# Kernel optimization log

Measured on AMD Instinct MI355X. Metric: run time of the kernel, lower is better.

Reference implementation:

```python
import jax, jax.numpy as jnp
import numpy as np

HIDDEN = 16
N_CLASSES = 10
N_NODES = 100000
N_EDGES = 3200000
D_FEAT = 128
NEG_SLOPE = 0.1


def setup_inputs() -> dict:
    key = jax.random.key(0)
    k1, k2, k3 = jax.random.split(key, 3)
    features = jax.random.normal(k1, (N_NODES, D_FEAT), dtype=jnp.float32)
    edge_src = jax.random.randint(k2, (N_EDGES,), 0, N_NODES, dtype=jnp.int64)
    edge_dst = jax.random.randint(k3, (N_EDGES,), 0, N_NODES, dtype=jnp.int64)
    return {"features": features, "edge_src": edge_src, "edge_dst": edge_dst}


def reference(features, edge_src, edge_dst):
    # SpMM: h[v] = sum over edges (u->v) of features[u]   (binary adjacency)
    msgs = features[edge_src]                      # [E, F] irregular gather
    h = jax.ops.segment_sum(msgs, edge_dst, num_segments=N_NODES)  # [N, F]
    # x @ ones(F, HIDDEN): every column equals the row-sum of h
    r1 = jnp.sum(h, axis=-1)                       # [N]
    a1 = jax.nn.leaky_relu(r1, NEG_SLOPE)          # leaky relu, slope 0.1
    # x @ ones(HIDDEN, N_CLASSES): each class column = HIDDEN * a1
    r2 = HIDDEN * a1
    a2 = jax.nn.leaky_relu(r2, NEG_SLOPE)
    # x @ ones(N_CLASSES, 1) then .int() and flatten
    r3 = N_CLASSES * a2                            # [N]
    return r3.astype(jnp.int32).reshape(-1)
```

## Files before the change

kernel.cpp:

```cpp
#include <hip/hip_runtime.h>

#define N_NODES  100000
#define N_EDGES  3200000
#define D_FEAT   128
#define SLICE    33344
#define SLICE4   (SLICE / 4)
#define N_SLICES 3
#define NCHUNK   80
#define EPB      40000
#define TPB      1024
#define STRIDE   (TPB * 8)

__device__ __forceinline__ unsigned short f2bf(float f) {
    union { float f; unsigned u; } c; c.f = f;
    unsigned r = c.u + 0x7FFFu + ((c.u >> 16) & 1u);
    return (unsigned short)(r >> 16);
}
__device__ __forceinline__ float bf2f(unsigned short h) {
    union { unsigned u; float f; } c; c.u = ((unsigned)h) << 16; return c.f;
}

__global__ void __launch_bounds__(256) rowsum_kernel(
    const float* __restrict__ feat,
    float* __restrict__ rowsum)
{
    const int gid = (int)(blockIdx.x * blockDim.x + threadIdx.x);
    const int row = gid >> 5;
    const int sub = gid & 31;
    if (row >= N_NODES) return;

    const float4 v = reinterpret_cast<const float4*>(
        feat + (size_t)row * D_FEAT)[sub];
    float s = (v.x + v.y) + (v.z + v.w);

    #pragma unroll
    for (int off = 16; off > 0; off >>= 1)
        s += __shfl_xor(s, off, 64);

    if (sub == 0) rowsum[row] = s;
}

__global__ void __launch_bounds__(256) gather_kernel(
    const int* __restrict__ edge_src,
    const float* __restrict__ rowsum,
    unsigned short* __restrict__ val)
{
    const int e = ((int)(blockIdx.x * 256 + threadIdx.x)) * 4;
    const int4 s4 = *reinterpret_cast<const int4*>(edge_src + e);
    ushort4 o;
    o.x = f2bf(rowsum[s4.x]);
    o.y = f2bf(rowsum[s4.y]);
    o.z = f2bf(rowsum[s4.z]);
    o.w = f2bf(rowsum[s4.w]);
    *reinterpret_cast<ushort4*>(val + e) = o;
}

__global__ void __launch_bounds__(TPB) scatter2_kernel(
    const int* __restrict__ edge_dst,
    const unsigned short* __restrict__ val,
    unsigned short* __restrict__ copies)
{
    __shared__ float lds[SLICE];

    const int tid = (int)threadIdx.x;
    const int bid = (int)blockIdx.x;
    const int g   = bid / 24;
    const int r   = bid % 24;
    const int xcd = r & 7;
    const int s   = r >> 3;
    const int b   = g * 8 + xcd;
    const int lo  = s * SLICE;
    const unsigned len = (unsigned)((N_NODES - lo < SLICE) ? (N_NODES - lo) : SLICE);

    float4 z; z.x = z.y = z.z = z.w = 0.0f;
    for (int i = tid; i < SLICE4; i += TPB)
        reinterpret_cast<float4*>(lds)[i] = z;
    __syncthreads();

    const int begin = b * EPB;
    const int end   = begin + EPB;

    int e = begin + tid * 8;
    bool v = (e < end);

    int4    d0, d1;
    ushort4 w01;
    ushort4 w23;
    if (v) {
        d0  = *(const int4*)(edge_dst + e);
        d1  = *(const int4*)(edge_dst + e + 4);
        w01 = *(const ushort4*)(val + e);
        w23 = *(const ushort4*)(val + e + 4);
    }

    while (v) {
        const int en = e + STRIDE;
        const bool vn = (en < end);
        int4 nd0, nd1; ushort4 nw01, nw23;
        if (vn) {
            nd0  = *(const int4*)(edge_dst + en);
            nd1  = *(const int4*)(edge_dst + en + 4);
            nw01 = *(const ushort4*)(val + en);
            nw23 = *(const ushort4*)(val + en + 4);
        }

        const unsigned j0 = (unsigned)(d0.x - lo);
        const unsigned j1 = (unsigned)(d0.y - lo);
        const unsigned j2 = (unsigned)(d0.z - lo);
        const unsigned j3 = (unsigned)(d0.w - lo);
        const unsigned j4 = (unsigned)(d1.x - lo);
        const unsigned j5 = (unsigned)(d1.y - lo);
        const unsigned j6 = (unsigned)(d1.z - lo);
        const unsigned j7 = (unsigned)(d1.w - lo);

        if (j0 < len) atomicAdd(&lds[j0], bf2f(w01.x));
        if (j1 < len) atomicAdd(&lds[j1], bf2f(w01.y));
        if (j2 < len) atomicAdd(&lds[j2], bf2f(w01.z));
        if (j3 < len) atomicAdd(&lds[j3], bf2f(w01.w));
        if (j4 < len) atomicAdd(&lds[j4], bf2f(w23.x));
        if (j5 < len) atomicAdd(&lds[j5], bf2f(w23.y));
        if (j6 < len) atomicAdd(&lds[j6], bf2f(w23.z));
        if (j7 < len) atomicAdd(&lds[j7], bf2f(w23.w));

        e = en; v = vn;
        d0 = nd0; d1 = nd1; w01 = nw01; w23 = nw23;
    }
    __syncthreads();

    unsigned short* __restrict__ dstp = copies + ((size_t)s * NCHUNK + b) * SLICE;
    const int len4 = (int)len >> 2;
    for (int i = tid; i < len4; i += TPB) {
        const float4 vv = reinterpret_cast<const float4*>(lds)[i];
        ushort4 o;
        o.x = f2bf(vv.x); o.y = f2bf(vv.y); o.z = f2bf(vv.z); o.w = f2bf(vv.w);
        reinterpret_cast<ushort4*>(dstp)[i] = o;
    }
}

__global__ void __launch_bounds__(256) reduce_final_kernel(
    const unsigned short* __restrict__ copies,
    int* __restrict__ out)
{
    const int i4 = (int)(blockIdx.x * blockDim.x + threadIdx.x);
    if (i4 >= N_NODES / 4) return;

    const int s  = (i4 >= 2 * SLICE4) ? 2 : (i4 >= SLICE4 ? 1 : 0);
    const int j4 = i4 - s * SLICE4;

    float ax = 0.0f, ay = 0.0f, az = 0.0f, aw = 0.0f;
    const ushort4* base = reinterpret_cast<const ushort4*>(copies)
                        + (size_t)s * NCHUNK * SLICE4 + j4;
    #pragma unroll 4
    for (int c = 0; c < NCHUNK; ++c) {
        const ushort4 v = base[(size_t)c * SLICE4];
        ax += bf2f(v.x); ay += bf2f(v.y); az += bf2f(v.z); aw += bf2f(v.w);
    }

    auto act = [](float x) -> int {
        const float a1 = (x  > 0.0f) ? x  : 0.1f * x;
        const float r2 = 16.0f * a1;
        const float a2 = (r2 > 0.0f) ? r2 : 0.1f * r2;
        return (int)(10.0f * a2);
    };

    int4 o;
    o.x = act(ax); o.y = act(ay); o.z = act(az); o.w = act(aw);
    reinterpret_cast<int4*>(out)[i4] = o;
}

extern "C" void kernel_launch(void* const* d_in, const int* in_sizes, int n_in,
                              void* d_out, int out_size, void* d_ws, size_t ws_size,
                              hipStream_t stream)
{
    const float* feat     = (const float*)d_in[0];
    const int*   edge_src = (const int*)d_in[1];
    const int*   edge_dst = (const int*)d_in[2];
    int*         out      = (int*)d_out;

    float* rowsum          = (float*)d_ws;
    unsigned short* val    = (unsigned short*)(rowsum + N_NODES);
    unsigned short* copies = val + N_EDGES;

    {
        const int threads = 256;
        const long long total = (long long)N_NODES * 32;
        const int blocks = (int)((total + threads - 1) / threads);
        rowsum_kernel<<<blocks, threads, 0, stream>>>(feat, rowsum);
    }

    gather_kernel<<<N_EDGES / (256 * 4), 256, 0, stream>>>(edge_src, rowsum, val);

    scatter2_kernel<<<N_SLICES * NCHUNK, TPB, 0, stream>>>(edge_dst, val, copies);

    {
        const int threads = 256;
        const int blocks = (N_NODES / 4 + threads - 1) / threads;
        reduce_final_kernel<<<blocks, threads, 0, stream>>>(copies, out);
    }
}
```

Baseline: 61.30 us.

## Stage bf16 rowsum table in LDS slices for edge gather

Rowsum is now stored as bf16, and the gather kernel copies the table into shared memory in four 25000-entry slices. Each 1024-thread block checks its 8 edges per thread against every slice, so lookups hit LDS instead of scattered global loads. In exchange, each block reloads the whole 200KB table from global/L2 and adds four barrier phases.

```diff
diff --git a/kernel.cpp b/kernel.cpp
--- a/kernel.cpp
+++ b/kernel.cpp
@@ -3,13 +3,21 @@
 #define N_NODES  100000
 #define N_EDGES  3200000
 #define D_FEAT   128
+
+#define G_TPB    1024
+#define G_EPT    8
+#define G_CHUNK  (G_TPB * G_EPT)
+#define G_GRID   ((N_EDGES + G_CHUNK - 1) / G_CHUNK)
+#define SRC_SLICE 25000
+#define N_SRC_SLICES 4
+
 #define SLICE    33344
 #define SLICE4   (SLICE / 4)
 #define N_SLICES 3
 #define NCHUNK   80
 #define EPB      40000
-#define TPB      1024
-#define STRIDE   (TPB * 8)
+#define S_TPB    1024
+#define S_STRIDE (S_TPB * 8)
 
 __device__ __forceinline__ unsigned short f2bf(float f) {
     union { float f; unsigned u; } c; c.f = f;
@@ -22,7 +30,7 @@
 
 __global__ void __launch_bounds__(256) rowsum_kernel(
     const float* __restrict__ feat,
-    float* __restrict__ rowsum)
+    unsigned short* __restrict__ rowsum_bf)
 {
     const int gid = (int)(blockIdx.x * blockDim.x + threadIdx.x);
     const int row = gid >> 5;
@@ -37,25 +45,55 @@
     for (int off = 16; off > 0; off >>= 1)
         s += __shfl_xor(s, off, 64);
 
-    if (sub == 0) rowsum[row] = s;
-}
-
-__global__ void __launch_bounds__(256) gather_kernel(
+    if (sub == 0) rowsum_bf[row] = f2bf(s);
+}
+
+__global__ void __launch_bounds__(G_TPB) gather_kernel(
     const int* __restrict__ edge_src,
-    const float* __restrict__ rowsum,
+    const unsigned short* __restrict__ rowsum_bf,
     unsigned short* __restrict__ val)
 {
-    const int e = ((int)(blockIdx.x * 256 + threadIdx.x)) * 4;
-    const int4 s4 = *reinterpret_cast<const int4*>(edge_src + e);
-    ushort4 o;
-    o.x = f2bf(rowsum[s4.x]);
-    o.y = f2bf(rowsum[s4.y]);
-    o.z = f2bf(rowsum[s4.z]);
-    o.w = f2bf(rowsum[s4.w]);
-    *reinterpret_cast<ushort4*>(val + e) = o;
-}
-
-__global__ void __launch_bounds__(TPB) scatter2_kernel(
+    __shared__ unsigned short tbl[SRC_SLICE];
+
+    const int tid  = (int)threadIdx.x;
+    const int base = (int)blockIdx.x * G_CHUNK + tid * G_EPT;
+    const bool v = (base + G_EPT) <= N_EDGES;
+
+    int4 s0 = {0,0,0,0}, s1 = {0,0,0,0};
+    if (v) {
+        s0 = *reinterpret_cast<const int4*>(edge_src + base);
+        s1 = *reinterpret_cast<const int4*>(edge_src + base + 4);
+    }
+
+    unsigned short w0 = 0, w1 = 0, w2 = 0, w3 = 0;
+    unsigned short w4 = 0, w5 = 0, w6 = 0, w7 = 0;
+
+    #pragma unroll
+    for (int p = 0; p < N_SRC_SLICES; ++p) {
+        const int lo = p * SRC_SLICE;
+
+        if (p > 0) __syncthreads();
+        for (int i = tid; i < SRC_SLICE / 4; i += G_TPB)
+            reinterpret_cast<uint2*>(tbl)[i] =
+                reinterpret_cast<const uint2*>(rowsum_bf + lo)[i];
+        __syncthreads();
+
+        #define GATHER1(S, W) { const unsigned j = (unsigned)((S) - lo); \
+                                if (j < SRC_SLICE) W = tbl[j]; }
+        GATHER1(s0.x, w0) GATHER1(s0.y, w1) GATHER1(s0.z, w2) GATHER1(s0.w, w3)
+        GATHER1(s1.x, w4) GATHER1(s1.y, w5) GATHER1(s1.z, w6) GATHER1(s1.w, w7)
+        #undef GATHER1
+    }
+
+    if (v) {
+        ushort4 o0; o0.x = w0; o0.y = w1; o0.z = w2; o0.w = w3;
+        ushort4 o1; o1.x = w4; o1.y = w5; o1.z = w6; o1.w = w7;
+        *reinterpret_cast<ushort4*>(val + base)     = o0;
+        *reinterpret_cast<ushort4*>(val + base + 4) = o1;
+    }
+}
+
+__global__ void __launch_bounds__(S_TPB) scatter2_kernel(
     const int* __restrict__ edge_dst,
     const unsigned short* __restrict__ val,
     unsigned short* __restrict__ copies)
@@ -73,7 +111,7 @@
     const unsigned len = (unsigned)((N_NODES - lo < SLICE) ? (N_NODES - lo) : SLICE);
 
     float4 z; z.x = z.y = z.z = z.w = 0.0f;
-    for (int i = tid; i < SLICE4; i += TPB)
+    for (int i = tid; i < SLICE4; i += S_TPB)
         reinterpret_cast<float4*>(lds)[i] = z;
     __syncthreads();
 
@@ -83,9 +121,7 @@
     int e = begin + tid * 8;
     bool v = (e < end);
 
-    int4    d0, d1;
-    ushort4 w01;
-    ushort4 w23;
+    int4 d0, d1; ushort4 w01, w23;
     if (v) {
         d0  = *(const int4*)(edge_dst + e);
         d1  = *(const int4*)(edge_dst + e + 4);
@@ -94,7 +130,7 @@
     }
 
     while (v) {
-        const int en = e + STRIDE;
+        const int en = e + S_STRIDE;
         const bool vn = (en < end);
         int4 nd0, nd1; ushort4 nw01, nw23;
         if (vn) {
@@ -129,7 +165,7 @@
 
     unsigned short* __restrict__ dstp = copies + ((size_t)s * NCHUNK + b) * SLICE;
     const int len4 = (int)len >> 2;
-    for (int i = tid; i < len4; i += TPB) {
+    for (int i = tid; i < len4; i += S_TPB) {
         const float4 vv = reinterpret_cast<const float4*>(lds)[i];
         ushort4 o;
         o.x = f2bf(vv.x); o.y = f2bf(vv.y); o.z = f2bf(vv.z); o.w = f2bf(vv.w);
@@ -177,20 +213,20 @@
     const int*   edge_dst = (const int*)d_in[2];
     int*         out      = (int*)d_out;
 
-    float* rowsum          = (float*)d_ws;
-    unsigned short* val    = (unsigned short*)(rowsum + N_NODES);
-    unsigned short* copies = val + N_EDGES;
+    unsigned short* rowsum_bf = (unsigned short*)d_ws;
+    unsigned short* val       = (unsigned short*)((char*)d_ws + (256 << 10));
+    unsigned short* copies    = val + N_EDGES;
 
     {
         const int threads = 256;
         const long long total = (long long)N_NODES * 32;
         const int blocks = (int)((total + threads - 1) / threads);
-        rowsum_kernel<<<blocks, threads, 0, stream>>>(feat, rowsum);
-    }
-
-    gather_kernel<<<N_EDGES / (256 * 4), 256, 0, stream>>>(edge_src, rowsum, val);
-
-    scatter2_kernel<<<N_SLICES * NCHUNK, TPB, 0, stream>>>(edge_dst, val, copies);
+        rowsum_kernel<<<blocks, threads, 0, stream>>>(feat, rowsum_bf);
+    }
+
+    gather_kernel<<<G_GRID, G_TPB, 0, stream>>>(edge_src, rowsum_bf, val);
+
+    scatter2_kernel<<<N_SLICES * NCHUNK, S_TPB, 0, stream>>>(edge_dst, val, copies);
 
     {
         const int threads = 256;
```

Measured after the change: 58.19 us. 1.05x faster.

## Fuse edge gather into sliced LDS scatter with two-deep prefetch

Applied to the files above, without the earlier changes.

Removes the separate gather kernel and its per-edge bf16 value buffer. Each scatter block now reads edge_src alongside edge_dst and gathers a bf16 row-sum only for edges whose destination falls in its slice. Row-sums are stored as bf16 (200KB) so the gathers stay cache-resident. A two-stage software pipeline issues index loads two iterations ahead and gathers one ahead to hide latency. The trade-off is that every one of the three slice blocks now reads edge_src, and the dependent gathers sit inside the scatter loop.

```diff
diff --git a/kernel.cpp b/kernel.cpp
--- a/kernel.cpp
+++ b/kernel.cpp
@@ -22,7 +22,7 @@
 
 __global__ void __launch_bounds__(256) rowsum_kernel(
     const float* __restrict__ feat,
-    float* __restrict__ rowsum)
+    unsigned short* __restrict__ rowsum_bf)
 {
     const int gid = (int)(blockIdx.x * blockDim.x + threadIdx.x);
     const int row = gid >> 5;
@@ -37,27 +37,13 @@
     for (int off = 16; off > 0; off >>= 1)
         s += __shfl_xor(s, off, 64);
 
-    if (sub == 0) rowsum[row] = s;
-}
-
-__global__ void __launch_bounds__(256) gather_kernel(
+    if (sub == 0) rowsum_bf[row] = f2bf(s);
+}
+
+__global__ void __launch_bounds__(TPB) scatter_kernel(
     const int* __restrict__ edge_src,
-    const float* __restrict__ rowsum,
-    unsigned short* __restrict__ val)
-{
-    const int e = ((int)(blockIdx.x * 256 + threadIdx.x)) * 4;
-    const int4 s4 = *reinterpret_cast<const int4*>(edge_src + e);
-    ushort4 o;
-    o.x = f2bf(rowsum[s4.x]);
-    o.y = f2bf(rowsum[s4.y]);
-    o.z = f2bf(rowsum[s4.z]);
-    o.w = f2bf(rowsum[s4.w]);
-    *reinterpret_cast<ushort4*>(val + e) = o;
-}
-
-__global__ void __launch_bounds__(TPB) scatter2_kernel(
     const int* __restrict__ edge_dst,
-    const unsigned short* __restrict__ val,
+    const unsigned short* __restrict__ rowsum_bf,
     unsigned short* __restrict__ copies)
 {
     __shared__ float lds[SLICE];
@@ -80,50 +66,82 @@
     const int begin = b * EPB;
     const int end   = begin + EPB;
 
-    int e = begin + tid * 8;
-    bool v = (e < end);
-
-    int4    d0, d1;
-    ushort4 w01;
-    ushort4 w23;
-    if (v) {
-        d0  = *(const int4*)(edge_dst + e);
-        d1  = *(const int4*)(edge_dst + e + 4);
-        w01 = *(const ushort4*)(val + e);
-        w23 = *(const ushort4*)(val + e + 4);
-    }
-
-    while (v) {
-        const int en = e + STRIDE;
-        const bool vn = (en < end);
-        int4 nd0, nd1; ushort4 nw01, nw23;
-        if (vn) {
-            nd0  = *(const int4*)(edge_dst + en);
-            nd1  = *(const int4*)(edge_dst + en + 4);
-            nw01 = *(const ushort4*)(val + en);
-            nw23 = *(const ushort4*)(val + en + 4);
+    int eA = begin + tid * 8;
+    int eB = eA + STRIDE;
+
+    int4 dA0, dA1, sA0, sA1, dB0, dB1, sB0, sB1;
+    if (eA < end) {
+        dA0 = *(const int4*)(edge_dst + eA);     sA0 = *(const int4*)(edge_src + eA);
+        dA1 = *(const int4*)(edge_dst + eA + 4); sA1 = *(const int4*)(edge_src + eA + 4);
+    }
+    if (eB < end) {
+        dB0 = *(const int4*)(edge_dst + eB);     sB0 = *(const int4*)(edge_src + eB);
+        dB1 = *(const int4*)(edge_dst + eB + 4); sB1 = *(const int4*)(edge_src + eB + 4);
+    }
+
+    unsigned jA0, jA1, jA2, jA3, jA4, jA5, jA6, jA7;
+    unsigned short wA0, wA1, wA2, wA3, wA4, wA5, wA6, wA7;
+    {
+        const bool v = (eA < end);
+        jA0 = v ? (unsigned)(dA0.x - lo) : 0xFFFFFFFFu;
+        jA1 = v ? (unsigned)(dA0.y - lo) : 0xFFFFFFFFu;
+        jA2 = v ? (unsigned)(dA0.z - lo) : 0xFFFFFFFFu;
+        jA3 = v ? (unsigned)(dA0.w - lo) : 0xFFFFFFFFu;
+        jA4 = v ? (unsigned)(dA1.x - lo) : 0xFFFFFFFFu;
+        jA5 = v ? (unsigned)(dA1.y - lo) : 0xFFFFFFFFu;
+        jA6 = v ? (unsigned)(dA1.z - lo) : 0xFFFFFFFFu;
+        jA7 = v ? (unsigned)(dA1.w - lo) : 0xFFFFFFFFu;
+        wA0 = (jA0 < len) ? rowsum_bf[sA0.x] : 0;
+        wA1 = (jA1 < len) ? rowsum_bf[sA0.y] : 0;
+        wA2 = (jA2 < len) ? rowsum_bf[sA0.z] : 0;
+        wA3 = (jA3 < len) ? rowsum_bf[sA0.w] : 0;
+        wA4 = (jA4 < len) ? rowsum_bf[sA1.x] : 0;
+        wA5 = (jA5 < len) ? rowsum_bf[sA1.y] : 0;
+        wA6 = (jA6 < len) ? rowsum_bf[sA1.z] : 0;
+        wA7 = (jA7 < len) ? rowsum_bf[sA1.w] : 0;
+    }
+
+    while (eA < end) {
+        const int eC = eB + STRIDE;
+        int4 dC0, dC1, sC0, sC1;
+        if (eC < end) {
+            dC0 = *(const int4*)(edge_dst + eC);     sC0 = *(const int4*)(edge_src + eC);
+            dC1 = *(const int4*)(edge_dst + eC + 4); sC1 = *(const int4*)(edge_src + eC + 4);
         }
 
-        const unsigned j0 = (unsigned)(d0.x - lo);
-        const unsigned j1 = (unsigned)(d0.y - lo);
-        const unsigned j2 = (unsigned)(d0.z - lo);
-        const unsigned j3 = (unsigned)(d0.w - lo);
-        const unsigned j4 = (unsigned)(d1.x - lo);
-        const unsigned j5 = (unsigned)(d1.y - lo);
-        const unsigned j6 = (unsigned)(d1.z - lo);
-        const unsigned j7 = (unsigned)(d1.w - lo);
-
-        if (j0 < len) atomicAdd(&lds[j0], bf2f(w01.x));
-        if (j1 < len) atomicAdd(&lds[j1], bf2f(w01.y));
-        if (j2 < len) atomicAdd(&lds[j2], bf2f(w01.z));
-        if (j3 < len) atomicAdd(&lds[j3], bf2f(w01.w));
-        if (j4 < len) atomicAdd(&lds[j4], bf2f(w23.x));
-        if (j5 < len) atomicAdd(&lds[j5], bf2f(w23.y));
-        if (j6 < len) atomicAdd(&lds[j6], bf2f(w23.z));
-        if (j7 < len) atomicAdd(&lds[j7], bf2f(w23.w));
-
-        e = en; v = vn;
-        d0 = nd0; d1 = nd1; w01 = nw01; w23 = nw23;
+        const bool v = (eB < end);
+        unsigned jB0 = v ? (unsigned)(dB0.x - lo) : 0xFFFFFFFFu;
+        unsigned jB1 = v ? (unsigned)(dB0.y - lo) : 0xFFFFFFFFu;
+        unsigned jB2 = v ? (unsigned)(dB0.z - lo) : 0xFFFFFFFFu;
+        unsigned jB3 = v ? (unsigned)(dB0.w - lo) : 0xFFFFFFFFu;
+        unsigned jB4 = v ? (unsigned)(dB1.x - lo) : 0xFFFFFFFFu;
+        unsigned jB5 = v ? (unsigned)(dB1.y - lo) : 0xFFFFFFFFu;
+        unsigned jB6 = v ? (unsigned)(dB1.z - lo) : 0xFFFFFFFFu;
+        unsigned jB7 = v ? (unsigned)(dB1.w - lo) : 0xFFFFFFFFu;
+        unsigned short wB0 = (jB0 < len) ? rowsum_bf[sB0.x] : 0;
+        unsigned short wB1 = (jB1 < len) ? rowsum_bf[sB0.y] : 0;
+        unsigned short wB2 = (jB2 < len) ? rowsum_bf[sB0.z] : 0;
+        unsigned short wB3 = (jB3 < len) ? rowsum_bf[sB0.w] : 0;
+        unsigned short wB4 = (jB4 < len) ? rowsum_bf[sB1.x] : 0;
+        unsigned short wB5 = (jB5 < len) ? rowsum_bf[sB1.y] : 0;
+        unsigned short wB6 = (jB6 < len) ? rowsum_bf[sB1.z] : 0;
+        unsigned short wB7 = (jB7 < len) ? rowsum_bf[sB1.w] : 0;
+
+        if (jA0 < len) atomicAdd(&lds[jA0], bf2f(wA0));
+        if (jA1 < len) atomicAdd(&lds[jA1], bf2f(wA1));
+        if (jA2 < len) atomicAdd(&lds[jA2], bf2f(wA2));
+        if (jA3 < len) atomicAdd(&lds[jA3], bf2f(wA3));
+        if (jA4 < len) atomicAdd(&lds[jA4], bf2f(wA4));
+        if (jA5 < len) atomicAdd(&lds[jA5], bf2f(wA5));
+        if (jA6 < len) atomicAdd(&lds[jA6], bf2f(wA6));
+        if (jA7 < len) atomicAdd(&lds[jA7], bf2f(wA7));
+
+        eA = eB; eB = eC;
+        dB0 = dC0; dB1 = dC1; sB0 = sC0; sB1 = sC1;
+        jA0 = jB0; jA1 = jB1; jA2 = jB2; jA3 = jB3;
+        jA4 = jB4; jA5 = jB5; jA6 = jB6; jA7 = jB7;
+        wA0 = wB0; wA1 = wB1; wA2 = wB2; wA3 = wB3;
+        wA4 = wB4; wA5 = wB5; wA6 = wB6; wA7 = wB7;
     }
     __syncthreads();
 
@@ -177,20 +195,19 @@
     const int*   edge_dst = (const int*)d_in[2];
     int*         out      = (int*)d_out;
 
-    float* rowsum          = (float*)d_ws;
-    unsigned short* val    = (unsigned short*)(rowsum + N_NODES);
-    unsigned short* copies = val + N_EDGES;
+    char* ws = (char*)d_ws;
+    unsigned short* rowsum_bf = (unsigned short*)(ws);
+    unsigned short* copies    = (unsigned short*)(ws + (256 << 10));
 
     {
         const int threads = 256;
         const long long total = (long long)N_NODES * 32;
         const int blocks = (int)((total + threads - 1) / threads);
-        rowsum_kernel<<<blocks, threads, 0, stream>>>(feat, rowsum);
-    }
-
-    gather_kernel<<<N_EDGES / (256 * 4), 256, 0, stream>>>(edge_src, rowsum, val);
-
-    scatter2_kernel<<<N_SLICES * NCHUNK, TPB, 0, stream>>>(edge_dst, val, copies);
+        rowsum_kernel<<<blocks, threads, 0, stream>>>(feat, rowsum_bf);
+    }
+
+    scatter_kernel<<<N_SLICES * NCHUNK, TPB, 0, stream>>>(edge_src, edge_dst,
+                                                          rowsum_bf, copies);
 
     {
         const int threads = 256;
```

Result: faster. 52.28 us (-14.7%).
